# Optimization experiments

Hardware: AMD Instinct MI355X
Metric: run time of the kernel (lower is better)

## Reference

```python
import jax, jax.numpy as jnp
import numpy as np

B, S, H = 2, 2048, 2048
NH, D_CKV, D_CQ, DR, DHV = 16, 512, 768, 64, 128
DH = H // NH            # 128 per-head content dim
SCALE = (DR + DH) ** -0.5


def apply_rope(x, freq):
    # x: [b, nh, s, d], freq: [s, d//2] angles; rotate interleaved pairs
    cos = jnp.cos(freq)
    sin = jnp.sin(freq)
    x1 = x[..., 0::2]
    x2 = x[..., 1::2]
    o1 = x1 * cos - x2 * sin
    o2 = x1 * sin + x2 * cos
    return jnp.stack([o1, o2], axis=-1).reshape(x.shape)


def setup_inputs() -> dict:
    key = jax.random.key(0)
    ks = jax.random.split(key, 16)
    w = lambda k, shape: jax.random.normal(k, shape, jnp.float32) * 0.02
    x = jax.random.normal(ks[0], (B, S, H), jnp.float32)
    # rotary angles: pos * inv_freq, shape [S, DR//2]
    inv = 1.0 / (10000.0 ** (jnp.arange(0, DR, 2, dtype=jnp.float32) / DR))
    freq = jnp.arange(S, dtype=jnp.float32)[:, None] * inv[None, :]
    mask = jnp.tril(jnp.ones((S, S), dtype=bool))[None, None]  # causal
    return {
        'x': x, 'freq': freq, 'mask': mask,
        'w_dq': w(ks[1], (H, D_CQ)),          'b_dq': jnp.zeros((D_CQ,), jnp.float32),
        'w_uq': w(ks[2], (D_CQ, NH * DH)),    'b_uq': jnp.zeros((NH * DH,), jnp.float32),
        'w_qr': w(ks[3], (D_CQ, NH * DR)),    'b_qr': jnp.zeros((NH * DR,), jnp.float32),
        'w_dkv': w(ks[4], (H, D_CKV)),        'b_dkv': jnp.zeros((D_CKV,), jnp.float32),
        'w_ukv': w(ks[5], (D_CKV, NH * (DH + DHV))), 'b_ukv': jnp.zeros((NH * (DH + DHV),), jnp.float32),
        'w_kr': w(ks[6], (H, DR)),            'b_kr': jnp.zeros((DR,), jnp.float32),
        'w_o': w(ks[7], (NH * DHV, H)),       'b_o': jnp.zeros((H,), jnp.float32),
    }


def reference(x, freq, mask, w_dq, b_dq, w_uq, b_uq, w_qr, b_qr,
              w_dkv, b_dkv, w_ukv, b_ukv, w_kr, b_kr, w_o, b_o):
    b, s, _ = x.shape
    # query branch: low-rank compression then up-projection
    c_q = x @ w_dq + b_dq                                   # [b,s,d_cq]
    q_c = (c_q @ w_uq + b_uq).reshape(b, s, NH, DH).transpose(0, 2, 1, 3)
    q_r = (c_q @ w_qr + b_qr).reshape(b, s, NH, DR).transpose(0, 2, 1, 3)
    q_r = apply_rope(q_r, freq)
    q = jnp.concatenate([q_c, q_r], axis=-1)               # [b,nh,s,dh+dr]
    # key/value branch: shared kv latent + shared rope key
    c_kv = x @ w_dkv + b_dkv                                # [b,s,d_ckv]
    kv_c = (c_kv @ w_ukv + b_ukv).reshape(b, s, NH, DH + DHV)
    k_c = kv_c[..., :DH].transpose(0, 2, 1, 3)              # [b,nh,s,dh]
    v_c = kv_c[..., DH:].transpose(0, 2, 1, 3)              # [b,nh,s,dhv]
    k_r = (x @ w_kr + b_kr).reshape(b, s, 1, DR).transpose(0, 2, 1, 3)
    k_r = apply_rope(k_r, freq)
    k_r = jnp.broadcast_to(k_r, (b, NH, s, DR))
    k = jnp.concatenate([k_c, k_r], axis=-1)               # [b,nh,s,dh+dr]
    # manual attention
    scores = jnp.einsum('bhsd,bhtd->bhst', q, k) * SCALE
    scores = jnp.where(mask, scores, -jnp.inf)
    attn = jax.nn.softmax(scores, axis=-1)
    out = jnp.einsum('bhst,bhtv->bhsv', attn, v_c)
    out = out.transpose(0, 2, 1, 3).reshape(b, s, NH * DHV)
    return out @ w_o + b_o
```

## Files before the change

### kernel.cpp

```cpp
#include <hip/hip_runtime.h>
#include <cstdint>
#include <cstddef>

#define S_LEN 2048
#define SCALE_F 0.07216878364870323f

typedef __attribute__((ext_vector_type(8))) short short8;
typedef __attribute__((ext_vector_type(4))) float f32x4;
typedef __attribute__((ext_vector_type(16))) float f32x16;
typedef __attribute__((ext_vector_type(4))) unsigned short ushort4v;

__device__ __forceinline__ unsigned short f2bf(float f) {
  unsigned int u = __builtin_bit_cast(unsigned int, f);
  u += 0x7FFFu + ((u >> 16) & 1u);
  return (unsigned short)(u >> 16);
}
__device__ __forceinline__ float bf2f(unsigned short h) {
  unsigned int u = ((unsigned int)h) << 16;
  return __builtin_bit_cast(float, u);
}
__device__ __forceinline__ unsigned int cvt_pk_bf16(float lo, float hi) {
  unsigned int r;
  asm("v_cvt_pk_bf16_f32 %0, %1, %2" : "=v"(r) : "v"(lo), "v"(hi));
  return r;
}

typedef const __attribute__((address_space(1))) void* gas_ptr;
typedef __attribute__((address_space(3))) void* las_ptr;
__device__ __forceinline__ void gload16(const void* g, void* l) {
  __builtin_amdgcn_global_load_lds((gas_ptr)g, (las_ptr)l, 16, 0, 0);
}


__device__ __forceinline__ void transpose_tile(
    const float* __restrict__ src, unsigned short* __restrict__ dst,
    int K, int N, int kb, int nb) {
  __shared__ __align__(16) unsigned short tile[64][72];
  const int tid = threadIdx.x;
  #pragma unroll
  for (int i = 0; i < 4; ++i) {
    int idx = i * 256 + tid;
    int row = idx >> 4, c4 = (idx & 15) << 2;
    const float4 v = *reinterpret_cast<const float4*>(&src[(size_t)(kb + row) * N + nb + c4]);
    tile[row][c4 + 0] = f2bf(v.x);
    tile[row][c4 + 1] = f2bf(v.y);
    tile[row][c4 + 2] = f2bf(v.z);
    tile[row][c4 + 3] = f2bf(v.w);
  }
  __syncthreads();
  #pragma unroll
  for (int i = 0; i < 4; ++i) {
    int idx = i * 256 + tid;
    int n = idx >> 4, kc = (idx & 15) << 2;
    ushort4v o = { tile[kc + 0][n], tile[kc + 1][n], tile[kc + 2][n], tile[kc + 3][n] };
    *reinterpret_cast<ushort4v*>(&dst[(size_t)(nb + n) * K + kb + kc]) = o;
  }
}

__global__ __launch_bounds__(256) void k_prep(
    const float* __restrict__ x, const float* __restrict__ freq,
    const float* __restrict__ wdq, const float* __restrict__ wdkv,
    const float* __restrict__ wkr, const float* __restrict__ wuq,
    const float* __restrict__ wqr, const float* __restrict__ wukv,
    const float* __restrict__ wo,
    const float* __restrict__ b_uq, const float* __restrict__ b_qr,
    const float* __restrict__ b_dq, const float* __restrict__ b_dkv,
    const float* __restrict__ b_kr,
    unsigned short* __restrict__ x_bf, unsigned short* __restrict__ wd_t,
    unsigned short* __restrict__ wqc_t, unsigned short* __restrict__ wukv_t,
    unsigned short* __restrict__ wo_t, float* __restrict__ tab,
    float* __restrict__ bcat, float* __restrict__ ball) {
  const int bid = blockIdx.x;
  const int tid = threadIdx.x;
  if (bid < 384) {
    transpose_tile(wdq, wd_t, 2048, 768, (bid / 12) << 6, (bid % 12) << 6);
  } else if (bid < 640) {
    int r = bid - 384;
    transpose_tile(wdkv, wd_t + (size_t)768 * 2048, 2048, 512, (r >> 3) << 6, (r & 7) << 6);
  } else if (bid < 672) {
    int r = bid - 640;
    transpose_tile(wkr, wd_t + (size_t)1280 * 2048, 2048, 64, r << 6, 0);
  } else if (bid < 1056) {
    int r = bid - 672;
    transpose_tile(wuq, wqc_t, 768, 2048, (r >> 5) << 6, (r & 31) << 6);
  } else if (bid < 1248) {
    int r = bid - 1056;
    transpose_tile(wqr, wqc_t + (size_t)2048 * 768, 768, 1024, (r >> 4) << 6, (r & 15) << 6);
  } else if (bid < 1760) {
    int r = bid - 1248;
    transpose_tile(wukv, wukv_t, 512, 4096, (r >> 6) << 6, (r & 63) << 6);
  } else if (bid < 2784) {
    int r = bid - 1760;
    transpose_tile(wo, wo_t, 2048, 2048, (r >> 5) << 6, (r & 31) << 6);
  } else if (bid < 10976) {
    int i = (bid - 2784) * 256 + tid;
    const float4 v = reinterpret_cast<const float4*>(x)[i];
    ushort4v o = { f2bf(v.x), f2bf(v.y), f2bf(v.z), f2bf(v.w) };
    reinterpret_cast<ushort4v*>(x_bf)[i] = o;
  } else if (bid < 11232) {
    int i = (bid - 10976) * 256 + tid;
    float f = freq[i];
    tab[2 * i] = cosf(f);
    tab[2 * i + 1] = sinf(f);
  } else {
    int i = (bid - 11232) * 256 + tid;
    if (i < 2048) bcat[i] = b_uq[i];
    else if (i < 3072) bcat[i] = b_qr[i - 2048];
    else if (i < 3840) ball[i - 3072] = b_dq[i - 3072];
    else if (i < 4352) ball[i - 3072] = b_dkv[i - 3840];
    else if (i < 4416) ball[i - 3072] = b_kr[i - 4352];
  }
}

__global__ void k_rope_kr(const unsigned short* __restrict__ src, int src_stride,
                          const float* __restrict__ tab,
                          unsigned short* __restrict__ out, int npairs) {
  int idx = blockIdx.x * 256 + threadIdx.x;
  if (idx >= npairs) return;
  int bs = idx >> 5, p = idx & 31;
  int s = bs & (S_LEN - 1);
  float c = tab[(s * 32 + p) * 2], sn = tab[(s * 32 + p) * 2 + 1];
  float x1 = bf2f(src[(size_t)bs * src_stride + 2 * p]);
  float x2 = bf2f(src[(size_t)bs * src_stride + 2 * p + 1]);
  out[bs * 64 + 2 * p] = f2bf(x1 * c - x2 * sn);
  out[bs * 64 + 2 * p + 1] = f2bf(x1 * sn + x2 * c);
}

template <int MODE>
__global__ __launch_bounds__(256) void k_gemm_bt(
    const unsigned short* __restrict__ A, const unsigned short* __restrict__ Bt,
    const float* __restrict__ bias, void* __restrict__ Cout,
    unsigned short* __restrict__ Vt, int M, int N, int K, int lda, int ldc) {
  __shared__ __align__(16) unsigned short SM[2 * 4096 + 2 * 4096];
  unsigned short* As = SM;
  unsigned short* Bs = SM + 2 * 4096;
  const int tid = threadIdx.x;
  const int lane = tid & 63, wid = tid >> 6;
  const int wr = wid >> 1, wc = wid & 1;
  const int nwg = gridDim.x * gridDim.y;
  const int id = blockIdx.y * gridDim.x + blockIdx.x;
  const int l = (id & 7) * (nwg >> 3) + (id >> 3);
  const int m0 = (l / gridDim.x) << 7, n0 = (l % gridDim.x) << 7;
  const int l15 = lane & 15, g = lane >> 4;

  const int srow = (wid << 5) + (lane >> 2);
  const int scol = (lane & 3) << 3;
  const unsigned short* aptr0 = &A[(size_t)(m0 + srow) * lda + scol];
  const unsigned short* aptr1 = &A[(size_t)(m0 + srow + 16) * lda + scol];
  int br0 = n0 + srow;      if (br0 >= N) br0 = N - 1;
  int br1 = n0 + srow + 16; if (br1 >= N) br1 = N - 1;
  const unsigned short* bptr0 = &Bt[(size_t)br0 * K + scol];
  const unsigned short* bptr1 = &Bt[(size_t)br1 * K + scol];
  const int lofs0 = ((wid << 1) + 0) << 9;
  const int lofs1 = ((wid << 1) + 1) << 9;

  f32x4 acc[4][4];
  #pragma unroll
  for (int m = 0; m < 4; ++m)
    #pragma unroll
    for (int n = 0; n < 4; ++n) acc[m][n] = f32x4{0.f, 0.f, 0.f, 0.f};

  gload16(aptr0, &As[lofs0]);
  gload16(aptr1, &As[lofs1]);
  gload16(bptr0, &Bs[lofs0]);
  gload16(bptr1, &Bs[lofs1]);
  __syncthreads();

  int cur = 0;
  for (int k0 = 0; k0 < K; k0 += 32) {
    const int nxt = cur ^ 1;
    if (k0 + 32 < K) {
      gload16(aptr0 + k0 + 32, &As[nxt * 4096 + lofs0]);
      gload16(aptr1 + k0 + 32, &As[nxt * 4096 + lofs1]);
      gload16(bptr0 + k0 + 32, &Bs[nxt * 4096 + lofs0]);
      gload16(bptr1 + k0 + 32, &Bs[nxt * 4096 + lofs1]);
    }
    short8 af[4], bfr[4];
    #pragma unroll
    for (int m = 0; m < 4; ++m)
      af[m] = *reinterpret_cast<const short8*>(
          &As[cur * 4096 + (((wr << 6) + (m << 4) + l15) << 5) + (g << 3)]);
    #pragma unroll
    for (int n = 0; n < 4; ++n)
      bfr[n] = *reinterpret_cast<const short8*>(
          &Bs[cur * 4096 + (((wc << 6) + (n << 4) + l15) << 5) + (g << 3)]);
    __builtin_amdgcn_s_setprio(1);
    #pragma unroll
    for (int m = 0; m < 4; ++m)
      #pragma unroll
      for (int n = 0; n < 4; ++n)
        acc[m][n] = __builtin_amdgcn_mfma_f32_16x16x32_bf16(af[m], bfr[n], acc[m][n], 0, 0, 0);
    __builtin_amdgcn_s_setprio(0);
    __syncthreads();
    cur = nxt;
  }

  if (MODE == 2 && (n0 & 128)) {
    const int hh = n0 >> 8;
    const int bb = m0 >> 11;
    const int s0 = m0 & 2047;
    unsigned short* T = SM;
    #pragma unroll
    for (int pass = 0; pass < 2; ++pass) {
      __syncthreads();
      if (wc == pass) {
        #pragma unroll
        for (int n = 0; n < 4; ++n) {
          int c = (n << 4) + l15;
          float bv = bias[n0 + (pass << 6) + c];
          #pragma unroll
          for (int m = 0; m < 4; ++m) {
            int rb = (wr << 6) + (m << 4) + (g << 2);
            #pragma unroll
            for (int r = 0; r < 4; ++r)
              T[c * 130 + rb + r] = f2bf(acc[m][n][r] + bv);
          }
        }
      }
      __syncthreads();
      int c = tid >> 2, seg = tid & 3;
      const unsigned short* src = &T[c * 130 + (seg << 5)];
      unsigned int wbuf[16];
      #pragma unroll
      for (int i = 0; i < 16; ++i)
        wbuf[i] = *reinterpret_cast<const unsigned int*>(&src[i * 2]);
      int4* dst = reinterpret_cast<int4*>(
          &Vt[(((size_t)bb * 16 + hh) * 128 + (pass << 6) + c) * 2048 + s0 + (seg << 5)]);
      #pragma unroll
      for (int i = 0; i < 4; ++i) {
        int4 v;
        v.x = (int)wbuf[4 * i + 0]; v.y = (int)wbuf[4 * i + 1];
        v.z = (int)wbuf[4 * i + 2]; v.w = (int)wbuf[4 * i + 3];
        dst[i] = v;
      }
    }
    return;
  }

  #pragma unroll
  for (int n = 0; n < 4; ++n) {
    int col = n0 + (wc << 6) + (n << 4) + l15;
    if (col >= N) continue;
    float bv = bias[col];
    #pragma unroll
    for (int m = 0; m < 4; ++m) {
      int rowb = m0 + (wr << 6) + (m << 4) + (g << 2);
      #pragma unroll
      for (int r = 0; r < 4; ++r) {
        float v = acc[m][n][r] + bv;
        int row = rowb + r;
        if (MODE == 0) {
          reinterpret_cast<float*>(Cout)[(size_t)row * ldc + col] = v;
        } else if (MODE == 1) {
          reinterpret_cast<unsigned short*>(Cout)[(size_t)row * ldc + col] = f2bf(v);
        } else {
          int hh = col >> 8, dd = col & 255;
          reinterpret_cast<unsigned short*>(Cout)[(size_t)row * 2048 + hh * 128 + dd] = f2bf(v);
        }
      }
    }
  }
}

__global__ __launch_bounds__(512, 2) void k_mla_attn(
    const unsigned short* __restrict__ q_raw, const unsigned short* __restrict__ kc,
    const unsigned short* __restrict__ v_t, const unsigned short* __restrict__ krro,
    const float* __restrict__ tab, unsigned short* __restrict__ attn_out) {
  __shared__ __align__(16) unsigned char smem[110592];
  unsigned short* KcB = reinterpret_cast<unsigned short*>(smem);
  unsigned short* VtB = reinterpret_cast<unsigned short*>(smem + 49152);
  float* Msh = reinterpret_cast<float*>(smem);

  const int tid = threadIdx.x;
  const int lane = tid & 63, w = tid >> 6;
  const int s = w & 3, e = w >> 2;
  const int l31 = lane & 31, hi = lane >> 5;
  const int hi8 = hi << 3;
  const int bid = blockIdx.x;
  const int bh = bid & 31, b = bh >> 4, h = bh & 15;
  const int uu = (bid >> 5) & 7;
  const int chunk = (bid >> 8) ? (15 - uu) : uu;
  const size_t bsb = (size_t)b * S_LEN;

  const int krow0 = (s << 3) + (lane >> 4);
  const int kunit = lane & 15;
  const int vd = (w << 4) + (lane >> 2);
  const int vu = lane & 3;
  const size_t vrow = ((size_t)(b * 16 + h) * 128 + vd) * 2048;

  const int q0 = (chunk << 7) + (s << 5);
  const int srow = q0 + l31;
  const int ntb = (chunk << 2) + 4;
  const int U = ntb >> 1;
  const int nt_w = (q0 + 63) >> 5;

  short8 qf[12];
  {
    const size_t qrow = (bsb + q0 + l31) * 3072;
    #pragma unroll
    for (int ks = 0; ks < 8; ++ks) {
      short8 rv = *reinterpret_cast<const short8*>(&q_raw[qrow + h * 128 + ks * 16 + hi8]);
      union { unsigned short us[8]; short8 v; } uq;
      #pragma unroll
      for (int j = 0; j < 8; ++j)
        uq.us[j] = f2bf(bf2f((unsigned short)rv[j]) * SCALE_F);
      qf[ks] = uq.v;
    }
    #pragma unroll
    for (int f = 0; f < 4; ++f) {
      short8 rv = *reinterpret_cast<const short8*>(
          &q_raw[qrow + 2048 + h * 64 + f * 16 + hi8]);
      int pi0 = 8 * f + 4 * hi;
      union { unsigned short us[8]; short8 v; } uq;
      #pragma unroll
      for (int j = 0; j < 4; ++j) {
        float c = tab[(srow * 32 + pi0 + j) * 2];
        float sn = tab[(srow * 32 + pi0 + j) * 2 + 1];
        float x1 = bf2f((unsigned short)rv[2 * j]);
        float x2 = bf2f((unsigned short)rv[2 * j + 1]);
        uq.us[2 * j] = f2bf((x1 * c - x2 * sn) * SCALE_F);
        uq.us[2 * j + 1] = f2bf((x1 * sn + x2 * c) * SCALE_F);
      }
      qf[8 + f] = uq.v;
    }
  }

  f32x16 acc[4];
  #pragma unroll
  for (int a = 0; a < 4; ++a)
    #pragma unroll
    for (int r = 0; r < 16; ++r) acc[a][r] = 0.f;
  float mrun = -1e30f, lsum = 0.f;

  short8 krf_cur[4], krf_nxt[4];
  int4 vcA, vcB;
  {
    #pragma unroll
    for (int f = 0; f < 4; ++f)
      krf_cur[f] = *reinterpret_cast<const short8*>(
          &krro[(bsb + e * 32 + l31) * 64 + f * 16 + hi8]);
    #pragma unroll
    for (int i = 0; i < 2; ++i) {
      const int ts = e + 2 * i;
      gload16(&kc[(bsb + (ts << 5) + krow0) * 2048 + h * 128 + (kunit ^ (krow0 & 15)) * 8],
              &KcB[(ts % 6) * 4096 + (krow0 << 7)]);
      gload16(&kc[(bsb + (ts << 5) + krow0 + 4) * 2048 + h * 128 + (kunit ^ ((krow0 + 4) & 15)) * 8],
              &KcB[(ts % 6) * 4096 + ((krow0 + 4) << 7)]);
    }
    #pragma unroll
    for (int tv = 0; tv < 4; ++tv) {
      int4 vv = *reinterpret_cast<const int4*>(&v_t[vrow + (tv << 5) + (vu << 3)]);
      *reinterpret_cast<int4*>(&VtB[tv * 5120 + vd * 40 + (vu << 3)]) = vv;
    }
    vcA = *reinterpret_cast<const int4*>(&v_t[vrow + (4 << 5) + (vu << 3)]);
    vcB = *reinterpret_cast<const int4*>(&v_t[vrow + (5 << 5) + (vu << 3)]);
  }
  __syncthreads();

  for (int u = 0; u < U; ++u) {
    const int t = (u << 1) + e;
    int tvA = (u << 1) + 6; int sA = tvA > 63 ? 63 : tvA;
    int tvB = tvA + 1;      int sB = tvB > 63 ? 63 : tvB;
    int4 vnA = *reinterpret_cast<const int4*>(&v_t[vrow + (sA << 5) + (vu << 3)]);
    int4 vnB = *reinterpret_cast<const int4*>(&v_t[vrow + (sB << 5) + (vu << 3)]);
    {
      int t2 = t + 2; if (t2 > 63) t2 = 63;
      #pragma unroll
      for (int f = 0; f < 4; ++f)
        krf_nxt[f] = *reinterpret_cast<const short8*>(
            &krro[(bsb + (t2 << 5) + l31) * 64 + f * 16 + hi8]);
    }
    {
      int tsK = (u << 1) + 4 + e;
      int src = tsK > 63 ? 63 : tsK;
      int kb = tsK % 6;
      gload16(&kc[(bsb + (src << 5) + krow0) * 2048 + h * 128 + (kunit ^ (krow0 & 15)) * 8],
              &KcB[kb * 4096 + (krow0 << 7)]);
      gload16(&kc[(bsb + (src << 5) + krow0 + 4) * 2048 + h * 128 + (kunit ^ ((krow0 + 4) & 15)) * 8],
              &KcB[kb * 4096 + ((krow0 + 4) << 7)]);
    }

    if (t < nt_w) {
      const int kvb = t << 5;
      const int kbuf = t % 6;

      f32x16 sca, scb;
      #pragma unroll
      for (int r = 0; r < 16; ++r) { sca[r] = 0.f; scb[r] = 0.f; }
      __builtin_amdgcn_s_setprio(1);
      #pragma unroll
      for (int j = 0; j < 4; ++j) {
        short8 k0 = *reinterpret_cast<const short8*>(
            &KcB[kbuf * 4096 + (l31 << 7) + ((((2 * (2 * j)) | hi) ^ (l31 & 15)) << 3)]);
        sca = __builtin_amdgcn_mfma_f32_32x32x16_bf16(k0, qf[2 * j], sca, 0, 0, 0);
        short8 k1 = *reinterpret_cast<const short8*>(
            &KcB[kbuf * 4096 + (l31 << 7) + ((((2 * (2 * j + 1)) | hi) ^ (l31 & 15)) << 3)]);
        scb = __builtin_amdgcn_mfma_f32_32x32x16_bf16(k1, qf[2 * j + 1], scb, 0, 0, 0);
      }
      sca = __builtin_amdgcn_mfma_f32_32x32x16_bf16(krf_cur[0], qf[8], sca, 0, 0, 0);
      scb = __builtin_amdgcn_mfma_f32_32x32x16_bf16(krf_cur[1], qf[9], scb, 0, 0, 0);
      sca = __builtin_amdgcn_mfma_f32_32x32x16_bf16(krf_cur[2], qf[10], sca, 0, 0, 0);
      scb = __builtin_amdgcn_mfma_f32_32x32x16_bf16(krf_cur[3], qf[11], scb, 0, 0, 0);
      __builtin_amdgcn_s_setprio(0);
      f32x16 sc = sca + scb;

      if (kvb + 31 > q0) {
        #pragma unroll
        for (int r = 0; r < 16; ++r) {
          int kv = kvb + (r & 3) + ((r >> 2) << 3) + (hi << 2);
          if (kv > srow) sc[r] = -1e30f;
        }
      }
      float m0 = fmaxf(fmaxf(sc[0], sc[1]), fmaxf(sc[2], sc[3]));
      float m1 = fmaxf(fmaxf(sc[4], sc[5]), fmaxf(sc[6], sc[7]));
      float m2 = fmaxf(fmaxf(sc[8], sc[9]), fmaxf(sc[10], sc[11]));
      float m3 = fmaxf(fmaxf(sc[12], sc[13]), fmaxf(sc[14], sc[15]));
      float tmax = fmaxf(fmaxf(m0, m1), fmaxf(m2, m3));
      tmax = fmaxf(tmax, __shfl_xor(tmax, 32));

      bool rescale = !__all(tmax <= mrun + 8.f);
      float scold = 1.f;
      if (rescale) {
        float mm = fmaxf(mrun, tmax);
        scold = __expf(mrun - mm);
        mrun = mm;
      }
      float pe[16];
      float ts = 0.f;
      #pragma unroll
      for (int r = 0; r < 16; ++r) { pe[r] = __expf(sc[r] - mrun); ts += pe[r]; }
      ts += __shfl_xor(ts, 32);
      lsum = lsum * scold + ts;

      if (rescale) {
        #pragma unroll
        for (int a = 0; a < 4; ++a)
          #pragma unroll
          for (int r = 0; r < 16; ++r) acc[a][r] *= scold;
      }
      #pragma unroll
      for (int ks = 0; ks < 2; ++ks) {
        unsigned int X0 = cvt_pk_bf16(pe[8 * ks + 0], pe[8 * ks + 1]);
        unsigned int X1 = cvt_pk_bf16(pe[8 * ks + 2], pe[8 * ks + 3]);
        unsigned int Y0 = cvt_pk_bf16(pe[8 * ks + 4], pe[8 * ks + 5]);
        unsigned int Y1 = cvt_pk_bf16(pe[8 * ks + 6], pe[8 * ks + 7]);
        unsigned int send0 = hi ? X0 : Y0;
        unsigned int send1 = hi ? X1 : Y1;
        unsigned int recv0 = (unsigned int)__shfl_xor((int)send0, 32);
        unsigned int recv1 = (unsigned int)__shfl_xor((int)send1, 32);
        union { unsigned int u[4]; short8 v; } pa;
        pa.u[0] = hi ? recv0 : X0;
        pa.u[1] = hi ? recv1 : X1;
        pa.u[2] = hi ? Y0 : recv0;
        pa.u[3] = hi ? Y1 : recv1;
        __builtin_amdgcn_s_setprio(1);
        #pragma unroll
        for (int a = 0; a < 4; ++a) {
          short8 va = *reinterpret_cast<const short8*>(
              &VtB[kbuf * 5120 + ((a << 5) + l31) * 40 + (((ks << 1) | hi) << 3)]);
          acc[a] = __builtin_amdgcn_mfma_f32_32x32x16_bf16(va, pa.v, acc[a], 0, 0, 0);
        }
        __builtin_amdgcn_s_setprio(0);
      }
    }

    *reinterpret_cast<int4*>(
        &VtB[(((u << 1) + 4) % 6) * 5120 + vd * 40 + (vu << 3)]) = vcA;
    *reinterpret_cast<int4*>(
        &VtB[(((u << 1) + 5) % 6) * 5120 + vd * 40 + (vu << 3)]) = vcB;
    vcA = vnA; vcB = vnB;
    #pragma unroll
    for (int f = 0; f < 4; ++f) krf_cur[f] = krf_nxt[f];
    asm volatile("s_waitcnt vmcnt(8) lgkmcnt(0)" ::: "memory");
    __builtin_amdgcn_s_barrier();
  }

  __syncthreads();

  if (e == 1) {
    #pragma unroll
    for (int a = 0; a < 4; ++a)
      #pragma unroll
      for (int r = 0; r < 16; ++r) {
        int v = 32 * a + (r & 3) + ((r >> 2) << 3) + (hi << 2);
        Msh[((s << 7) + v) * 33 + l31] = acc[a][r];
      }
    if (hi == 0) {
      Msh[16896 + ((s << 5) + l31) * 2 + 0] = mrun;
      Msh[16896 + ((s << 5) + l31) * 2 + 1] = lsum;
    }
  }
  __syncthreads();
  if (e == 0) {
    float m1 = Msh[16896 + ((s << 5) + l31) * 2 + 0];
    float l1 = Msh[16896 + ((s << 5) + l31) * 2 + 1];
    float mm = fmaxf(mrun, m1);
    float ea = __expf(mrun - mm), eb = __expf(m1 - mm);
    float linv = 1.f / (lsum * ea + l1 * eb);
    float al = ea * linv, be = eb * linv;
    #pragma unroll
    for (int a = 0; a < 4; ++a)
      #pragma unroll
      for (int r = 0; r < 16; ++r) {
        int v = 32 * a + (r & 3) + ((r >> 2) << 3) + (hi << 2);
        float part = Msh[((s << 7) + v) * 33 + l31];
        acc[a][r] = acc[a][r] * al + part * be;
      }
    unsigned int* Tb = reinterpret_cast<unsigned int*>(smem) + s * 4224;
    #pragma unroll
    for (int a = 0; a < 4; ++a)
      #pragma unroll
      for (int j = 0; j < 8; ++j) {
        unsigned int word = cvt_pk_bf16(acc[a][2 * j], acc[a][2 * j + 1]);
        int wc = 16 * a + 2 * hi + (j & 1) + 4 * (j >> 1);
        Tb[l31 * 68 + wc] = word;
      }
    const unsigned char* Tbb = reinterpret_cast<const unsigned char*>(Tb);
    #pragma unroll
    for (int u2 = 0; u2 < 8; ++u2) {
      int qr = (u2 << 2) + (lane >> 4);
      int4 rd = *reinterpret_cast<const int4*>(&Tbb[qr * 272 + (lane & 15) * 16]);
      *reinterpret_cast<int4*>(
          &attn_out[(bsb + q0 + qr) * 2048 + h * 128 + (lane & 15) * 8]) = rd;
    }
  }
}


extern "C" void kernel_launch(void* const* d_in, const int* in_sizes, int n_in,
                              void* d_out, int out_size, void* d_ws, size_t ws_size,
                              hipStream_t stream) {
  (void)in_sizes; (void)n_in; (void)out_size; (void)ws_size;
  const float* x = (const float*)d_in[0];
  const float* freq = (const float*)d_in[1];
  const float* w_dq = (const float*)d_in[3];
  const float* b_dq = (const float*)d_in[4];
  const float* w_uq = (const float*)d_in[5];
  const float* b_uq = (const float*)d_in[6];
  const float* w_qr = (const float*)d_in[7];
  const float* b_qr = (const float*)d_in[8];
  const float* w_dkv = (const float*)d_in[9];
  const float* b_dkv = (const float*)d_in[10];
  const float* w_ukv = (const float*)d_in[11];
  const float* b_ukv = (const float*)d_in[12];
  const float* w_kr = (const float*)d_in[13];
  const float* b_kr = (const float*)d_in[14];
  const float* w_o = (const float*)d_in[15];
  const float* b_o = (const float*)d_in[16];

  char* ws = (char*)d_ws;
  size_t off = 0;
  auto alloc = [&](size_t bytes) {
    char* p = ws + off;
    off += (bytes + 255) & ~(size_t)255;
    return p;
  };
  unsigned short* x_bf   = (unsigned short*)alloc((size_t)4096 * 2048 * 2);
  unsigned short* wd_t   = (unsigned short*)alloc((size_t)1344 * 2048 * 2);
  unsigned short* wqc_t  = (unsigned short*)alloc((size_t)3072 * 768 * 2);
  unsigned short* wukv_t = (unsigned short*)alloc((size_t)4096 * 512 * 2);
  unsigned short* wo_t   = (unsigned short*)alloc((size_t)2048 * 2048 * 2);
  float* tab             = (float*)alloc((size_t)2048 * 32 * 2 * 4);
  float* bcat            = (float*)alloc((size_t)3072 * 4);
  float* ball            = (float*)alloc((size_t)1344 * 4);
  unsigned short* c_all  = (unsigned short*)alloc((size_t)4096 * 1344 * 2);
  unsigned short* krro   = (unsigned short*)alloc((size_t)4096 * 64 * 2);
  unsigned short* q_raw  = (unsigned short*)alloc((size_t)4096 * 3072 * 2);
  unsigned short* kc     = (unsigned short*)alloc((size_t)4096 * 2048 * 2);
  unsigned short* v_t    = (unsigned short*)alloc((size_t)4096 * 2048 * 2);
  unsigned short* attn   = (unsigned short*)alloc((size_t)4096 * 2048 * 2);

  k_prep<<<dim3(11250), dim3(256), 0, stream>>>(
      x, freq, w_dq, w_dkv, w_kr, w_uq, w_qr, w_ukv, w_o,
      b_uq, b_qr, b_dq, b_dkv, b_kr,
      x_bf, wd_t, wqc_t, wukv_t, wo_t, tab, bcat, ball);

  k_gemm_bt<1><<<dim3(11, 32), dim3(256), 0, stream>>>(
      x_bf, wd_t, ball, c_all, nullptr, 4096, 1344, 2048, 2048, 1344);
  k_rope_kr<<<dim3(512), dim3(256), 0, stream>>>(c_all + 1280, 1344, tab, krro, 4096 * 32);

  k_gemm_bt<1><<<dim3(24, 32), dim3(256), 0, stream>>>(
      c_all, wqc_t, bcat, q_raw, nullptr, 4096, 3072, 768, 1344, 3072);
  k_gemm_bt<2><<<dim3(32, 32), dim3(256), 0, stream>>>(
      c_all + 768, wukv_t, b_ukv, kc, v_t, 4096, 4096, 512, 1344, 2048);

  k_mla_attn<<<dim3(512), dim3(512), 0, stream>>>(q_raw, kc, v_t, krro, tab, attn);

  k_gemm_bt<0><<<dim3(16, 32), dim3(256), 0, stream>>>(
      attn, wo_t, b_o, (float*)d_out, nullptr, 4096, 2048, 2048, 2048, 2048);
}
```

Measured before the change: 259.3 us.

## Merge launches into heterogeneous kernels overlapping weight transposes with GEMMs, use exp2

Splits the prep kernel so that only the weights needed by the down-projection are transposed first. The remaining weight transposes are co-scheduled as extra blocks inside the down-projection GEMM launch. The Q and KV up-projection GEMMs and the k_r rope are merged into one launch, and the GEMM becomes a device body indexed by sub-block id. The attention softmax folds log2(e) into the query scale and uses exp2f instead of __expf. The goal is fewer launches, better fill of idle CUs, and cheaper exponentials. The cost is that merged kernels carry the largest shared-memory footprint for all blocks, and block types are imbalanced within each launch.

```diff
diff --git a/kernel.cpp b/kernel.cpp
--- a/kernel.cpp
+++ b/kernel.cpp
@@ -3,7 +3,7 @@
 #include <cstddef>
 
 #define S_LEN 2048
-#define SCALE_F 0.07216878364870323f
+#define SCALE_L2E (0.07216878364870323f * 1.4426950408889634f)
 
 typedef __attribute__((ext_vector_type(8))) short short8;
 typedef __attribute__((ext_vector_type(4))) float f32x4;
@@ -34,113 +34,42 @@
 
 __device__ __forceinline__ void transpose_tile(
     const float* __restrict__ src, unsigned short* __restrict__ dst,
-    int K, int N, int kb, int nb) {
-  __shared__ __align__(16) unsigned short tile[64][72];
+    int K, int N, int kb, int nb, unsigned short* tile) {
   const int tid = threadIdx.x;
   #pragma unroll
   for (int i = 0; i < 4; ++i) {
     int idx = i * 256 + tid;
     int row = idx >> 4, c4 = (idx & 15) << 2;
     const float4 v = *reinterpret_cast<const float4*>(&src[(size_t)(kb + row) * N + nb + c4]);
-    tile[row][c4 + 0] = f2bf(v.x);
-    tile[row][c4 + 1] = f2bf(v.y);
-    tile[row][c4 + 2] = f2bf(v.z);
-    tile[row][c4 + 3] = f2bf(v.w);
+    tile[row * 72 + c4 + 0] = f2bf(v.x);
+    tile[row * 72 + c4 + 1] = f2bf(v.y);
+    tile[row * 72 + c4 + 2] = f2bf(v.z);
+    tile[row * 72 + c4 + 3] = f2bf(v.w);
   }
   __syncthreads();
   #pragma unroll
   for (int i = 0; i < 4; ++i) {
     int idx = i * 256 + tid;
     int n = idx >> 4, kc = (idx & 15) << 2;
-    ushort4v o = { tile[kc + 0][n], tile[kc + 1][n], tile[kc + 2][n], tile[kc + 3][n] };
+    ushort4v o = { tile[(kc + 0) * 72 + n], tile[(kc + 1) * 72 + n],
+                   tile[(kc + 2) * 72 + n], tile[(kc + 3) * 72 + n] };
     *reinterpret_cast<ushort4v*>(&dst[(size_t)(nb + n) * K + kb + kc]) = o;
   }
 }
 
-__global__ __launch_bounds__(256) void k_prep(
-    const float* __restrict__ x, const float* __restrict__ freq,
-    const float* __restrict__ wdq, const float* __restrict__ wdkv,
-    const float* __restrict__ wkr, const float* __restrict__ wuq,
-    const float* __restrict__ wqr, const float* __restrict__ wukv,
-    const float* __restrict__ wo,
-    const float* __restrict__ b_uq, const float* __restrict__ b_qr,
-    const float* __restrict__ b_dq, const float* __restrict__ b_dkv,
-    const float* __restrict__ b_kr,
-    unsigned short* __restrict__ x_bf, unsigned short* __restrict__ wd_t,
-    unsigned short* __restrict__ wqc_t, unsigned short* __restrict__ wukv_t,
-    unsigned short* __restrict__ wo_t, float* __restrict__ tab,
-    float* __restrict__ bcat, float* __restrict__ ball) {
-  const int bid = blockIdx.x;
-  const int tid = threadIdx.x;
-  if (bid < 384) {
-    transpose_tile(wdq, wd_t, 2048, 768, (bid / 12) << 6, (bid % 12) << 6);
-  } else if (bid < 640) {
-    int r = bid - 384;
-    transpose_tile(wdkv, wd_t + (size_t)768 * 2048, 2048, 512, (r >> 3) << 6, (r & 7) << 6);
-  } else if (bid < 672) {
-    int r = bid - 640;
-    transpose_tile(wkr, wd_t + (size_t)1280 * 2048, 2048, 64, r << 6, 0);
-  } else if (bid < 1056) {
-    int r = bid - 672;
-    transpose_tile(wuq, wqc_t, 768, 2048, (r >> 5) << 6, (r & 31) << 6);
-  } else if (bid < 1248) {
-    int r = bid - 1056;
-    transpose_tile(wqr, wqc_t + (size_t)2048 * 768, 768, 1024, (r >> 4) << 6, (r & 15) << 6);
-  } else if (bid < 1760) {
-    int r = bid - 1248;
-    transpose_tile(wukv, wukv_t, 512, 4096, (r >> 6) << 6, (r & 63) << 6);
-  } else if (bid < 2784) {
-    int r = bid - 1760;
-    transpose_tile(wo, wo_t, 2048, 2048, (r >> 5) << 6, (r & 31) << 6);
-  } else if (bid < 10976) {
-    int i = (bid - 2784) * 256 + tid;
-    const float4 v = reinterpret_cast<const float4*>(x)[i];
-    ushort4v o = { f2bf(v.x), f2bf(v.y), f2bf(v.z), f2bf(v.w) };
-    reinterpret_cast<ushort4v*>(x_bf)[i] = o;
-  } else if (bid < 11232) {
-    int i = (bid - 10976) * 256 + tid;
-    float f = freq[i];
-    tab[2 * i] = cosf(f);
-    tab[2 * i + 1] = sinf(f);
-  } else {
-    int i = (bid - 11232) * 256 + tid;
-    if (i < 2048) bcat[i] = b_uq[i];
-    else if (i < 3072) bcat[i] = b_qr[i - 2048];
-    else if (i < 3840) ball[i - 3072] = b_dq[i - 3072];
-    else if (i < 4352) ball[i - 3072] = b_dkv[i - 3840];
-    else if (i < 4416) ball[i - 3072] = b_kr[i - 4352];
-  }
-}
-
-__global__ void k_rope_kr(const unsigned short* __restrict__ src, int src_stride,
-                          const float* __restrict__ tab,
-                          unsigned short* __restrict__ out, int npairs) {
-  int idx = blockIdx.x * 256 + threadIdx.x;
-  if (idx >= npairs) return;
-  int bs = idx >> 5, p = idx & 31;
-  int s = bs & (S_LEN - 1);
-  float c = tab[(s * 32 + p) * 2], sn = tab[(s * 32 + p) * 2 + 1];
-  float x1 = bf2f(src[(size_t)bs * src_stride + 2 * p]);
-  float x2 = bf2f(src[(size_t)bs * src_stride + 2 * p + 1]);
-  out[bs * 64 + 2 * p] = f2bf(x1 * c - x2 * sn);
-  out[bs * 64 + 2 * p + 1] = f2bf(x1 * sn + x2 * c);
-}
-
 template <int MODE>
-__global__ __launch_bounds__(256) void k_gemm_bt(
+__device__ __forceinline__ void gemm_body(
     const unsigned short* __restrict__ A, const unsigned short* __restrict__ Bt,
     const float* __restrict__ bias, void* __restrict__ Cout,
-    unsigned short* __restrict__ Vt, int M, int N, int K, int lda, int ldc) {
-  __shared__ __align__(16) unsigned short SM[2 * 4096 + 2 * 4096];
+    unsigned short* __restrict__ Vt, int N, int K, int lda, int ldc,
+    int subId, int subN, int gx, unsigned short* SM) {
   unsigned short* As = SM;
-  unsigned short* Bs = SM + 2 * 4096;
+  unsigned short* Bs = SM + 8192;
   const int tid = threadIdx.x;
   const int lane = tid & 63, wid = tid >> 6;
   const int wr = wid >> 1, wc = wid & 1;
-  const int nwg = gridDim.x * gridDim.y;
-  const int id = blockIdx.y * gridDim.x + blockIdx.x;
-  const int l = (id & 7) * (nwg >> 3) + (id >> 3);
-  const int m0 = (l / gridDim.x) << 7, n0 = (l % gridDim.x) << 7;
+  const int l = (subId & 7) * (subN >> 3) + (subId >> 3);
+  const int m0 = (l / gx) << 7, n0 = (l % gx) << 7;
   const int l15 = lane & 15, g = lane >> 4;
 
   const int srow = (wid << 5) + (lane >> 2);
@@ -262,6 +191,110 @@
   }
 }
 
+
+__global__ __launch_bounds__(256) void k_prep_a(
+    const float* __restrict__ x, const float* __restrict__ freq,
+    const float* __restrict__ wdq, const float* __restrict__ wdkv,
+    const float* __restrict__ wkr,
+    const float* __restrict__ b_uq, const float* __restrict__ b_qr,
+    const float* __restrict__ b_dq, const float* __restrict__ b_dkv,
+    const float* __restrict__ b_kr,
+    unsigned short* __restrict__ x_bf, unsigned short* __restrict__ wd_t,
+    float* __restrict__ tab, float* __restrict__ bcat, float* __restrict__ ball) {
+  __shared__ __align__(16) unsigned short SMEM[64 * 72];
+  const int bid = blockIdx.x;
+  const int tid = threadIdx.x;
+  if (bid < 384) {
+    transpose_tile(wdq, wd_t, 2048, 768, (bid / 12) << 6, (bid % 12) << 6, SMEM);
+  } else if (bid < 640) {
+    int r = bid - 384;
+    transpose_tile(wdkv, wd_t + (size_t)768 * 2048, 2048, 512, (r >> 3) << 6, (r & 7) << 6, SMEM);
+  } else if (bid < 672) {
+    int r = bid - 640;
+    transpose_tile(wkr, wd_t + (size_t)1280 * 2048, 2048, 64, r << 6, 0, SMEM);
+  } else if (bid < 8864) {
+    int i = (bid - 672) * 256 + tid;
+    const float4 v = reinterpret_cast<const float4*>(x)[i];
+    ushort4v o = { f2bf(v.x), f2bf(v.y), f2bf(v.z), f2bf(v.w) };
+    reinterpret_cast<ushort4v*>(x_bf)[i] = o;
+  } else if (bid < 9120) {
+    int i = (bid - 8864) * 256 + tid;
+    float f = freq[i];
+    tab[2 * i] = cosf(f);
+    tab[2 * i + 1] = sinf(f);
+  } else {
+    int i = (bid - 9120) * 256 + tid;
+    if (i < 2048) bcat[i] = b_uq[i];
+    else if (i < 3072) bcat[i] = b_qr[i - 2048];
+    else if (i < 3840) ball[i - 3072] = b_dq[i - 3072];
+    else if (i < 4352) ball[i - 3072] = b_dkv[i - 3840];
+    else if (i < 4416) ball[i - 3072] = b_kr[i - 4352];
+  }
+}
+
+__global__ __launch_bounds__(256) void k_down(
+    const unsigned short* __restrict__ x_bf, const unsigned short* __restrict__ wd_t,
+    const float* __restrict__ ball, unsigned short* __restrict__ c_all,
+    const float* __restrict__ wuq, const float* __restrict__ wqr,
+    const float* __restrict__ wukv, const float* __restrict__ wo,
+    unsigned short* __restrict__ wqc_t, unsigned short* __restrict__ wukv_t,
+    unsigned short* __restrict__ wo_t) {
+  __shared__ __align__(16) unsigned short SMEM[16384];
+  const int bid = blockIdx.x;
+  if (bid < 352) {
+    gemm_body<1>(x_bf, wd_t, ball, c_all, nullptr, 1344, 2048, 2048, 1344,
+                 bid, 352, 11, SMEM);
+  } else if (bid < 736) {
+    int r = bid - 352;
+    transpose_tile(wuq, wqc_t, 768, 2048, (r >> 5) << 6, (r & 31) << 6, SMEM);
+  } else if (bid < 928) {
+    int r = bid - 736;
+    transpose_tile(wqr, wqc_t + (size_t)2048 * 768, 768, 1024, (r >> 4) << 6, (r & 15) << 6, SMEM);
+  } else if (bid < 1440) {
+    int r = bid - 928;
+    transpose_tile(wukv, wukv_t, 512, 4096, (r >> 6) << 6, (r & 63) << 6, SMEM);
+  } else {
+    int r = bid - 1440;
+    transpose_tile(wo, wo_t, 2048, 2048, (r >> 5) << 6, (r & 31) << 6, SMEM);
+  }
+}
+
+__global__ __launch_bounds__(256) void k_up(
+    const unsigned short* __restrict__ c_all, const unsigned short* __restrict__ wqc_t,
+    const float* __restrict__ bcat, unsigned short* __restrict__ q_raw,
+    const unsigned short* __restrict__ wukv_t, const float* __restrict__ b_ukv,
+    unsigned short* __restrict__ kc, unsigned short* __restrict__ v_t,
+    const float* __restrict__ tab, unsigned short* __restrict__ krro) {
+  __shared__ __align__(16) unsigned short SMEM[16384];
+  const int bid = blockIdx.x;
+  if (bid < 768) {
+    gemm_body<1>(c_all, wqc_t, bcat, q_raw, nullptr, 3072, 768, 1344, 3072,
+                 bid, 768, 24, SMEM);
+  } else if (bid < 1792) {
+    gemm_body<2>(c_all + 768, wukv_t, b_ukv, kc, v_t, 4096, 512, 1344, 2048,
+                 bid - 768, 1024, 32, SMEM);
+  } else {
+    int idx = (bid - 1792) * 256 + threadIdx.x;
+    if (idx < 4096 * 32) {
+      int bs = idx >> 5, p = idx & 31;
+      int s = bs & (S_LEN - 1);
+      float c = tab[(s * 32 + p) * 2], sn = tab[(s * 32 + p) * 2 + 1];
+      float x1 = bf2f(c_all[(size_t)bs * 1344 + 1280 + 2 * p]);
+      float x2 = bf2f(c_all[(size_t)bs * 1344 + 1280 + 2 * p + 1]);
+      krro[bs * 64 + 2 * p] = f2bf(x1 * c - x2 * sn);
+      krro[bs * 64 + 2 * p + 1] = f2bf(x1 * sn + x2 * c);
+    }
+  }
+}
+
+__global__ __launch_bounds__(256) void k_out(
+    const unsigned short* __restrict__ attn, const unsigned short* __restrict__ wo_t,
+    const float* __restrict__ b_o, float* __restrict__ out) {
+  __shared__ __align__(16) unsigned short SMEM[16384];
+  gemm_body<0>(attn, wo_t, b_o, out, nullptr, 2048, 2048, 2048, 2048,
+               (int)blockIdx.x, 512, 16, SMEM);
+}
+
 __global__ __launch_bounds__(512, 2) void k_mla_attn(
     const unsigned short* __restrict__ q_raw, const unsigned short* __restrict__ kc,
     const unsigned short* __restrict__ v_t, const unsigned short* __restrict__ krro,
@@ -303,7 +336,7 @@
       union { unsigned short us[8]; short8 v; } uq;
       #pragma unroll
       for (int j = 0; j < 8; ++j)
-        uq.us[j] = f2bf(bf2f((unsigned short)rv[j]) * SCALE_F);
+        uq.us[j] = f2bf(bf2f((unsigned short)rv[j]) * SCALE_L2E);
       qf[ks] = uq.v;
     }
     #pragma unroll
@@ -318,8 +351,8 @@
         float sn = tab[(srow * 32 + pi0 + j) * 2 + 1];
         float x1 = bf2f((unsigned short)rv[2 * j]);
         float x2 = bf2f((unsigned short)rv[2 * j + 1]);
-        uq.us[2 * j] = f2bf((x1 * c - x2 * sn) * SCALE_F);
-        uq.us[2 * j + 1] = f2bf((x1 * sn + x2 * c) * SCALE_F);
+        uq.us[2 * j] = f2bf((x1 * c - x2 * sn) * SCALE_L2E);
+        uq.us[2 * j + 1] = f2bf((x1 * sn + x2 * c) * SCALE_L2E);
       }
       qf[8 + f] = uq.v;
     }
@@ -422,13 +455,13 @@
       float scold = 1.f;
       if (rescale) {
         float mm = fmaxf(mrun, tmax);
-        scold = __expf(mrun - mm);
+        scold = exp2f(mrun - mm);
         mrun = mm;
       }
       float pe[16];
       float ts = 0.f;
       #pragma unroll
-      for (int r = 0; r < 16; ++r) { pe[r] = __expf(sc[r] - mrun); ts += pe[r]; }
+      for (int r = 0; r < 16; ++r) { pe[r] = exp2f(sc[r] - mrun); ts += pe[r]; }
       ts += __shfl_xor(ts, 32);
       lsum = lsum * scold + ts;
 
@@ -495,7 +528,7 @@
     float m1 = Msh[16896 + ((s << 5) + l31) * 2 + 0];
     float l1 = Msh[16896 + ((s << 5) + l31) * 2 + 1];
     float mm = fmaxf(mrun, m1);
-    float ea = __expf(mrun - mm), eb = __expf(m1 - mm);
+    float ea = exp2f(mrun - mm), eb = exp2f(m1 - mm);
     float linv = 1.f / (lsum * ea + l1 * eb);
     float al = ea * linv, be = eb * linv;
     #pragma unroll
@@ -570,22 +603,17 @@
   unsigned short* v_t    = (unsigned short*)alloc((size_t)4096 * 2048 * 2);
   unsigned short* attn   = (unsigned short*)alloc((size_t)4096 * 2048 * 2);
 
-  k_prep<<<dim3(11250), dim3(256), 0, stream>>>(
-      x, freq, w_dq, w_dkv, w_kr, w_uq, w_qr, w_ukv, w_o,
-      b_uq, b_qr, b_dq, b_dkv, b_kr,
-      x_bf, wd_t, wqc_t, wukv_t, wo_t, tab, bcat, ball);
-
-  k_gemm_bt<1><<<dim3(11, 32), dim3(256), 0, stream>>>(
-      x_bf, wd_t, ball, c_all, nullptr, 4096, 1344, 2048, 2048, 1344);
-  k_rope_kr<<<dim3(512), dim3(256), 0, stream>>>(c_all + 1280, 1344, tab, krro, 4096 * 32);
-
-  k_gemm_bt<1><<<dim3(24, 32), dim3(256), 0, stream>>>(
-      c_all, wqc_t, bcat, q_raw, nullptr, 4096, 3072, 768, 1344, 3072);
-  k_gemm_bt<2><<<dim3(32, 32), dim3(256), 0, stream>>>(
-      c_all + 768, wukv_t, b_ukv, kc, v_t, 4096, 4096, 512, 1344, 2048);
+  k_prep_a<<<dim3(9138), dim3(256), 0, stream>>>(
+      x, freq, w_dq, w_dkv, w_kr, b_uq, b_qr, b_dq, b_dkv, b_kr,
+      x_bf, wd_t, tab, bcat, ball);
+
+  k_down<<<dim3(2464), dim3(256), 0, stream>>>(
+      x_bf, wd_t, ball, c_all, w_uq, w_qr, w_ukv, w_o, wqc_t, wukv_t, wo_t);
+
+  k_up<<<dim3(2304), dim3(256), 0, stream>>>(
+      c_all, wqc_t, bcat, q_raw, wukv_t, b_ukv, kc, v_t, tab, krro);
 
   k_mla_attn<<<dim3(512), dim3(512), 0, stream>>>(q_raw, kc, v_t, krro, tab, attn);
 
-  k_gemm_bt<0><<<dim3(16, 32), dim3(256), 0, stream>>>(
-      attn, wo_t, b_o, (float*)d_out, nullptr, 4096, 2048, 2048, 2048, 2048);
-}
+  k_out<<<dim3(512), dim3(256), 0, stream>>>(attn, wo_t, b_o, (float*)d_out);
+}
```

Result: no change. 256.8 us (-1.0%).
